# Performance work log

Hardware: AMD Instinct MI355X
Metric: run time of the kernel (lower is better)

## Reference

```python
import jax, jax.numpy as jnp
import numpy as np

B = 1024
D = 64          # embed_dim (symp == dise)
H1, H2 = 8, 8   # dsd metapath fanouts
U1, U2, U3 = 8, 8, 16  # usu metapath fanouts
NUM_SYMP = 50000
NUM_DISE = 2000
NEG_SLOPE = 0.2


def setup_inputs() -> dict:
    key = jax.random.key(0)
    ks = jax.random.split(key, 16)
    s = 0.05
    E_s = jax.random.normal(ks[0], (NUM_SYMP + 1, D), jnp.float32) * s
    E_d = jax.random.normal(ks[1], (NUM_DISE + 1, D), jnp.float32) * s
    # padding_idx=0 rows are zero in torch Embedding
    E_s = E_s.at[0].set(0.0)
    E_d = E_d.at[0].set(0.0)
    W = lambda k: jax.random.normal(k, (D, D), jnp.float32) * (1.0 / np.sqrt(D))
    return {
        "E_s": E_s,
        "E_d": E_d,
        "W_dsd_21": W(ks[2]),
        "W_dsd_22": W(ks[3]),
        "W_dsd_11": W(ks[4]),
        "W_dsd_12": W(ks[5]),
        "W_usu_3": W(ks[6]),
        "W_usu_21": W(ks[7]),
        "W_usu_22": W(ks[8]),
        "W_usu_1": W(ks[9]),
        "label": jax.random.randint(ks[10], (B,), 0, NUM_DISE + 1),
        "dsd_1": jax.random.randint(ks[11], (B, H1), 0, NUM_SYMP + 1),
        "dsd_2": jax.random.randint(ks[12], (B, H1, H2), 0, NUM_DISE + 1),
        "usu_1": jax.random.randint(ks[13], (B, U1), 0, NUM_SYMP + 1),
        "usu_2": jax.random.randint(ks[14], (B, U1, U2), 0, 10000),
        "usu_3": jax.random.randint(ks[15], (B, U1, U2, U3), 0, NUM_SYMP + 1),
    }


def _avg_real(msg, idx):
    # mean over the neighbor axis, counting only nonzero (real) neighbors;
    # zero output if all neighbors are padding (matches weight==1e8 -> 0)
    cnt = (idx != 0).sum(-1).astype(msg.dtype)
    w = jnp.where(cnt > 0, 1.0 / (cnt + 1e-8), 0.0)
    return msg.sum(-2) * w[..., None]


def _leaky(x):
    return jax.nn.leaky_relu(x, NEG_SLOPE)


def reference(E_s, E_d, W_dsd_21, W_dsd_22, W_dsd_11, W_dsd_12,
              W_usu_3, W_usu_21, W_usu_22, W_usu_1,
              label, dsd_1, dsd_2, usu_1, usu_2, usu_3):
    # ---- forward_dsd (eval mode: dropout = identity) ----
    td = E_d[label]                       # [B, D]
    es = E_s[dsd_1]                       # [B, H1, D]
    ed = E_d[dsd_2]                       # [B, H1, H2, D]
    m_sd = ed @ W_dsd_21.T + (ed * es[:, :, None, :]) @ W_dsd_22.T
    m_sd = _avg_real(m_sd, dsd_2)         # [B, H1, D]
    m_ss = es @ W_dsd_21.T                # [B, H1, D]
    emb_s1 = _leaky(m_ss + m_sd)          # [B, H1, D]
    m_ds = emb_s1 @ W_dsd_11.T + (emb_s1 * td[:, None, :]) @ W_dsd_12.T
    m_ds = _avg_real(m_ds, dsd_1)         # [B, D]
    emb_dise = _leaky(m_ds + td @ W_dsd_11.T)

    # ---- forward_usu ----
    u1 = E_s[usu_1]                       # [B, U1, D]
    s3 = E_s[usu_3]                       # [B, U1, U2, U3, D]
    m_us3 = _avg_real(s3 @ W_usu_3.T, usu_3)   # [B, U1, U2, D]
    eu2 = _leaky(m_us3)                   # [B, U1, U2, D]
    m_su = eu2 @ W_usu_21.T + (eu2 * u1[:, :, None, :]) @ W_usu_22.T
    m_su = _avg_real(m_su, usu_2)         # [B, U1, D]
    m_ss_u = u1 @ W_usu_21.T              # [B, U1, D]
    es1 = _leaky(m_ss_u + m_su)           # [B, U1, D]
    emb_user = _leaky(_avg_real(es1 @ W_usu_1.T, usu_1))  # [B, D]

    pred_score = (emb_dise * emb_user).sum(-1)  # [B]
    return pred_score
```

## Files before the change

kernel.cpp:

```cpp
#include <hip/hip_runtime.h>
#include <hip/hip_bf16.h>


typedef __attribute__((ext_vector_type(8))) short short8;
typedef __attribute__((ext_vector_type(8))) unsigned short ushort8;
typedef __attribute__((ext_vector_type(4))) float f32x4;

__device__ __forceinline__ int rfl(int v) { return __builtin_amdgcn_readfirstlane(v); }
__device__ __forceinline__ float bcastf(float v, int l) {
    return __int_as_float(__builtin_amdgcn_readlane(__float_as_int(v), l));
}
__device__ __forceinline__ float leakyf(float x) { return x >= 0.f ? x : 0.2f * x; }

__device__ __forceinline__ unsigned short bf16bits(float x) {
    __hip_bfloat16 h = __float2bfloat16(x);
    return __builtin_bit_cast(unsigned short, h);
}
__device__ __forceinline__ float bflo(unsigned int u) { return __uint_as_float(u << 16); }
__device__ __forceinline__ float bfhi(unsigned int u) { return __uint_as_float(u & 0xffff0000u); }

__device__ __forceinline__ void stage_w512(float* dst, const float* __restrict__ W, int tid) {
#pragma unroll
    for (int c = 0; c < 2; ++c) {
        int f4 = c * 512 + tid;
        int j = f4 >> 4, g = f4 & 15;
        float4 v = reinterpret_cast<const float4*>(W)[f4];
        reinterpret_cast<float4*>(dst)[(j << 4) + ((g + j) & 15)] = v;
    }
}

__device__ __forceinline__ float dot1_lds(float x, const float* w, int lane) {
    float a0 = 0.f, a1 = 0.f, a2 = 0.f, a3 = 0.f;
#pragma unroll
    for (int g = 0; g < 16; ++g) {
        float4 c = reinterpret_cast<const float4*>(w)[(lane << 4) + ((g + lane) & 15)];
        int k = 4 * g;
        a0 = fmaf(bcastf(x, k + 0), c.x, a0);
        a1 = fmaf(bcastf(x, k + 1), c.y, a1);
        a2 = fmaf(bcastf(x, k + 2), c.z, a2);
        a3 = fmaf(bcastf(x, k + 3), c.w, a3);
    }
    return (a0 + a1) + (a2 + a3);
}

__global__ __launch_bounds__(256) void k_cvt(const float* __restrict__ E_s,
                                             unsigned short* __restrict__ T) {
    int t = blockIdx.x * 256 + threadIdx.x;
    if (t >= 400008) return;
    const float4* p = reinterpret_cast<const float4*>(E_s) + (size_t)t * 2;
    float4 a = p[0], b = p[1];
    ushort8 o;
    o[0] = bf16bits(a.x); o[1] = bf16bits(a.y); o[2] = bf16bits(a.z); o[3] = bf16bits(a.w);
    o[4] = bf16bits(b.x); o[5] = bf16bits(b.y); o[6] = bf16bits(b.z); o[7] = bf16bits(b.w);
    *(reinterpret_cast<ushort8*>(T) + t) = o;
}

#define XP 72

__device__ __forceinline__ f32x4 pair_mfma(
    const unsigned short* sXs, const unsigned short* sXm,
    const unsigned short* sWb1, const unsigned short* sWb2,
    int arow, int brow, int quad)
{
    const int ab = arow * XP + quad * 8;
    const int bb = brow * XP + quad * 8;
    short8 as0 = *(const short8*)(sXs + ab);
    short8 as1 = *(const short8*)(sXs + ab + 32);
    short8 am0 = *(const short8*)(sXm + ab);
    short8 am1 = *(const short8*)(sXm + ab + 32);
    short8 b10 = *(const short8*)(sWb1 + bb);
    short8 b11 = *(const short8*)(sWb1 + bb + 32);
    short8 b20 = *(const short8*)(sWb2 + bb);
    short8 b21 = *(const short8*)(sWb2 + bb + 32);
    f32x4 acc = {0.f, 0.f, 0.f, 0.f};
    acc = __builtin_amdgcn_mfma_f32_16x16x32_bf16(as0, b10, acc, 0, 0, 0);
    acc = __builtin_amdgcn_mfma_f32_16x16x32_bf16(as1, b11, acc, 0, 0, 0);
    acc = __builtin_amdgcn_mfma_f32_16x16x32_bf16(am0, b20, acc, 0, 0, 0);
    acc = __builtin_amdgcn_mfma_f32_16x16x32_bf16(am1, b21, acc, 0, 0, 0);
    return acc;
}

__global__ __launch_bounds__(512, 6) void k_main(
    const float* __restrict__ E_s, const unsigned short* __restrict__ Ebf,
    const float* __restrict__ E_d,
    const float* __restrict__ W21, const float* __restrict__ W22,
    const float* __restrict__ W11, const float* __restrict__ W12,
    const float* __restrict__ W3, const float* __restrict__ W21u,
    const float* __restrict__ W22u, const float* __restrict__ W1u,
    const int* __restrict__ label, const int* __restrict__ dsd_1,
    const int* __restrict__ dsd_2, const int* __restrict__ usu_1,
    const int* __restrict__ usu_2, const int* __restrict__ usu_3,
    float* __restrict__ emb_dise, float* __restrict__ emb_user)
{
    __shared__ float4 smraw[2560];
    const int tid = threadIdx.x, lane = tid & 63, w = rfl(tid >> 6);
    const int m_ = lane & 15, quad = lane >> 4;

    if (blockIdx.x < 1024) {
        const int b = blockIdx.x;
        unsigned short* sXb   = (unsigned short*)smraw;
        unsigned short* sW3b  = sXb + 4608;
        unsigned short* sW21b = sW3b + 4608;
        unsigned short* sW22b = sW21b + 4608;
        float* sA2  = (float*)(sW22b + 4608);
        float* sES1 = sA2 + 512;
        unsigned short* sXs = sXb;
        unsigned short* sXm = sXb + 16 * XP;

        const int sub = lane >> 4, cg = lane & 15;

        int idv[8];
#pragma unroll
        for (int i = 0; i < 8; ++i)
            idv[i] = usu_3[((size_t)(b * 64 + w * 8 + i)) * 16 + cg];

        {
            int row = tid >> 3, c0 = (tid & 7) << 3;
            const float* p3 = W3 + row * 64 + c0;
            const float* p1 = W21u + row * 64 + c0;
            const float* p2 = W22u + row * 64 + c0;
#pragma unroll
            for (int i = 0; i < 8; ++i) {
                sW3b[row * XP + c0 + i]  = bf16bits(p3[i]);
                sW21b[row * XP + c0 + i] = bf16bits(p1[i]);
                sW22b[row * XP + c0 + i] = bf16bits(p2[i]);
            }
        }

#pragma unroll 2
        for (int i = 0; i < 8; ++i) {
            int ql = w * 8 + i;
            unsigned long long nzm = __ballot(idv[i] != 0) & 0xFFFFull;
            int cnt = (int)__popcll(nzm);
            float wgt = cnt > 0 ? 1.f / ((float)cnt + 1e-8f) : 0.f;
            float a0 = 0.f, a1 = 0.f, a2 = 0.f, a3 = 0.f;
#pragma unroll
            for (int k = 0; k < 4; ++k) {
                int id = __shfl(idv[i], k * 4 + sub, 64);
                uint2 v = *reinterpret_cast<const uint2*>(Ebf + (size_t)id * 64 + cg * 4);
                a0 += bflo(v.x); a1 += bfhi(v.x);
                a2 += bflo(v.y); a3 += bfhi(v.y);
            }
            a0 += __shfl_xor(a0, 16, 64); a1 += __shfl_xor(a1, 16, 64);
            a2 += __shfl_xor(a2, 16, 64); a3 += __shfl_xor(a3, 16, 64);
            a0 += __shfl_xor(a0, 32, 64); a1 += __shfl_xor(a1, 32, 64);
            a2 += __shfl_xor(a2, 32, 64); a3 += __shfl_xor(a3, 32, 64);
            a0 *= wgt; a1 *= wgt; a2 *= wgt; a3 *= wgt;
            unsigned int p0 = ((unsigned int)bf16bits(a1) << 16) | bf16bits(a0);
            unsigned int p1 = ((unsigned int)bf16bits(a3) << 16) | bf16bits(a2);
            if (sub == 0) {
                uint2 st; st.x = p0; st.y = p1;
                *reinterpret_cast<uint2*>(sXb + ql * XP + cg * 4) = st;
            }
        }
        __syncthreads();

        {
            const int wt = w >> 1, J0 = (w & 1) * 2;
            const int base = (16 * wt + m_) * XP + quad * 8;
            short8 a0 = *(const short8*)(sXb + base);
            short8 a1 = *(const short8*)(sXb + base + 32);
            int cp0 = 0, cp1 = 0;
            const int* m2 = usu_2 + (b * 8 + 2 * wt) * 8;
#pragma unroll
            for (int u = 0; u < 8; ++u) { cp0 += (m2[u] != 0); cp1 += (m2[u + 8] != 0); }
            float wg0 = cp0 > 0 ? 1.f / ((float)cp0 + 1e-8f) : 0.f;
            float wg1 = cp1 > 0 ? 1.f / ((float)cp1 + 1e-8f) : 0.f;
#pragma unroll
            for (int jj = 0; jj < 2; ++jj) {
                int J = J0 + jj;
                const int wb = (16 * J + m_) * XP + quad * 8;
                short8 b0 = *(const short8*)(sW3b + wb);
                short8 b1 = *(const short8*)(sW3b + wb + 32);
                f32x4 acc = {0.f, 0.f, 0.f, 0.f};
                acc = __builtin_amdgcn_mfma_f32_16x16x32_bf16(a0, b0, acc, 0, 0, 0);
                acc = __builtin_amdgcn_mfma_f32_16x16x32_bf16(a1, b1, acc, 0, 0, 0);
                float t = leakyf(acc[0]) + leakyf(acc[1]) + leakyf(acc[2]) + leakyf(acc[3]);
                t += __shfl_xor(t, 16, 64);
                if (quad == 0) sA2[(2 * wt + 0) * 64 + J * 16 + m_] = t * wg0;
                if (quad == 2) sA2[(2 * wt + 1) * 64 + J * 16 + m_] = t * wg1;
            }
        }
        __syncthreads();

        {
            int p = w;
            float x = sA2[p * 64 + lane];
            float u1e = E_s[(size_t)usu_1[b * 8 + p] * 64 + lane];
            sXs[p * XP + lane] = bf16bits(x + u1e);
            sXm[p * XP + lane] = bf16bits(x * u1e);
        }
        __syncthreads();

        if (w < 4) {
            f32x4 acc = pair_mfma(sXs, sXm, sW21b, sW22b, m_, 16 * w + m_, quad);
            if (quad < 2) {
#pragma unroll
                for (int r = 0; r < 4; ++r)
                    sES1[(quad * 4 + r) * 64 + w * 16 + m_] = leakyf(acc[r]);
            }
        }
        __syncthreads();

        stage_w512((float*)sW21b, W1u, tid);
        __syncthreads();

        if (w == 0) {
            float sE = 0.f; int cnt = 0;
            const int* u1i = usu_1 + b * 8;
#pragma unroll
            for (int h = 0; h < 8; ++h) {
                sE += sES1[h * 64 + lane];
                cnt += (u1i[h] != 0);
            }
            float wgt = cnt > 0 ? 1.f / ((float)cnt + 1e-8f) : 0.f;
            float eu = leakyf(dot1_lds(sE * wgt, (float*)sW21b, lane));
            emb_user[(size_t)b * 64 + lane] = eu;
        }
    } else {
        const int b0 = (blockIdx.x - 1024) * 4;
        unsigned short* sXs   = (unsigned short*)smraw;
        unsigned short* sXm   = sXs + 2304;
        unsigned short* sW21b = sXm + 2304;
        unsigned short* sW22b = sW21b + 4608;
        float* sS1 = (float*)(sW22b + 4608);

        {
            int row = tid >> 3, c0 = (tid & 7) << 3;
            const float* p1 = W21 + row * 64 + c0;
            const float* p2 = W22 + row * 64 + c0;
#pragma unroll
            for (int i = 0; i < 8; ++i) {
                sW21b[row * XP + c0 + i] = bf16bits(p1[i]);
                sW22b[row * XP + c0 + i] = bf16bits(p2[i]);
            }
        }

#pragma unroll
        for (int i = 0; i < 4; ++i) {
            int rl = w * 4 + i;
            int row = b0 * 8 + rl;
            int is = dsd_1[row];
            float es = E_s[(size_t)is * 64 + lane];
            const int* d2 = dsd_2 + row * 8;
            float sA = 0.f; int cnt = 0;
#pragma unroll
            for (int h = 0; h < 8; ++h) {
                int id = d2[h];
                cnt += (id != 0);
                sA += E_d[(size_t)id * 64 + lane];
            }
            float wgt = cnt > 0 ? 1.f / ((float)cnt + 1e-8f) : 0.f;
            float A = sA * wgt;
            sXs[rl * XP + lane] = bf16bits(A + es);
            sXm[rl * XP + lane] = bf16bits(A * es);
        }
        __syncthreads();

        {
            const int Mt = w >> 2, J = w & 3;
            f32x4 acc = pair_mfma(sXs, sXm, sW21b, sW22b,
                                  16 * Mt + m_, 16 * J + m_, quad);
#pragma unroll
            for (int r = 0; r < 4; ++r)
                sS1[(16 * Mt + quad * 4 + r) * 64 + J * 16 + m_] = leakyf(acc[r]);
        }
        __syncthreads();

        if (w < 4) {
            int bb = b0 + w;
            float sE = 0.f; int cnt = 0;
            const int* d1 = dsd_1 + bb * 8;
#pragma unroll
            for (int h = 0; h < 8; ++h) {
                sE += sS1[(w * 8 + h) * 64 + lane];
                cnt += (d1[h] != 0);
            }
            float wgt = cnt > 0 ? 1.f / ((float)cnt + 1e-8f) : 0.f;
            float A3 = sE * wgt;
            float td = E_d[(size_t)label[bb] * 64 + lane];
            sXs[w * XP + lane] = bf16bits(A3 + td);
            sXm[w * XP + lane] = bf16bits(A3 * td);
        } else {
            int t2 = tid - 256;
            int row = t2 >> 2, c0 = (t2 & 3) << 4;
            const float* p1 = W11 + row * 64 + c0;
            const float* p2 = W12 + row * 64 + c0;
#pragma unroll
            for (int i = 0; i < 16; ++i) {
                sW21b[row * XP + c0 + i] = bf16bits(p1[i]);
                sW22b[row * XP + c0 + i] = bf16bits(p2[i]);
            }
        }
        __syncthreads();

        if (w < 4) {
            f32x4 acc = pair_mfma(sXs, sXm, sW21b, sW22b, m_, 16 * w + m_, quad);
            if (quad == 0) {
#pragma unroll
                for (int r = 0; r < 4; ++r)
                    emb_dise[(size_t)(b0 + r) * 64 + w * 16 + m_] = leakyf(acc[r]);
            }
        }
    }
}

__global__ __launch_bounds__(256) void k_dot(const float* __restrict__ ed,
                                             const float* __restrict__ eu,
                                             float* __restrict__ out) {
    const int lane = threadIdx.x & 63;
    const int b = rfl((int)((blockIdx.x * blockDim.x + threadIdx.x) >> 6));
    float pr = ed[(size_t)b * 64 + lane] * eu[(size_t)b * 64 + lane];
#pragma unroll
    for (int off = 32; off > 0; off >>= 1) pr += __shfl_down(pr, off, 64);
    if (lane == 0) out[b] = pr;
}

extern "C" void kernel_launch(void* const* d_in, const int* in_sizes, int n_in,
                              void* d_out, int out_size, void* d_ws, size_t ws_size,
                              hipStream_t stream) {
    const float* E_s  = (const float*)d_in[0];
    const float* E_d  = (const float*)d_in[1];
    const float* W_dsd_21 = (const float*)d_in[2];
    const float* W_dsd_22 = (const float*)d_in[3];
    const float* W_dsd_11 = (const float*)d_in[4];
    const float* W_dsd_12 = (const float*)d_in[5];
    const float* W_usu_3  = (const float*)d_in[6];
    const float* W_usu_21 = (const float*)d_in[7];
    const float* W_usu_22 = (const float*)d_in[8];
    const float* W_usu_1  = (const float*)d_in[9];
    const int* label = (const int*)d_in[10];
    const int* dsd_1 = (const int*)d_in[11];
    const int* dsd_2 = (const int*)d_in[12];
    const int* usu_1 = (const int*)d_in[13];
    const int* usu_2 = (const int*)d_in[14];
    const int* usu_3 = (const int*)d_in[15];
    float* out = (float*)d_out;

    unsigned short* Ebf = (unsigned short*)d_ws;
    float* emb_dise = (float*)((char*)d_ws + 6400128);
    float* emb_user = emb_dise + 1024 * 64;

    k_cvt<<<1563, 256, 0, stream>>>(E_s, Ebf);
    k_main<<<1280, 512, 0, stream>>>(E_s, Ebf, E_d,
                                     W_dsd_21, W_dsd_22, W_dsd_11, W_dsd_12,
                                     W_usu_3, W_usu_21, W_usu_22, W_usu_1,
                                     label, dsd_1, dsd_2, usu_1, usu_2, usu_3,
                                     emb_dise, emb_user);
    k_dot<<<256, 256, 0, stream>>>(emb_dise, emb_user, out);
}
```

Measured before the change: 115.6 us.

## Restructure usu block: per-wave W3 MFMA, bf16 W1u staging, MFMA final projection

The usu branch now stages W1u as bf16 in LDS up front instead of restaging fp32 W1u over W21 late. Each wave runs the W3 MFMA on its own eight gathered rows with a wave-local count, removing one block barrier. The final emb_user projection uses an MFMA on four waves in place of the single-wave readlane dot product. This raises LDS use per block, which may lower occupancy, and rounds the final projection to bf16.

```diff
diff --git a/kernel.cpp b/kernel.cpp
--- a/kernel.cpp
+++ b/kernel.cpp
@@ -7,9 +7,6 @@
 typedef __attribute__((ext_vector_type(4))) float f32x4;
 
 __device__ __forceinline__ int rfl(int v) { return __builtin_amdgcn_readfirstlane(v); }
-__device__ __forceinline__ float bcastf(float v, int l) {
-    return __int_as_float(__builtin_amdgcn_readlane(__float_as_int(v), l));
-}
 __device__ __forceinline__ float leakyf(float x) { return x >= 0.f ? x : 0.2f * x; }
 
 __device__ __forceinline__ unsigned short bf16bits(float x) {
@@ -18,30 +15,6 @@
 }
 __device__ __forceinline__ float bflo(unsigned int u) { return __uint_as_float(u << 16); }
 __device__ __forceinline__ float bfhi(unsigned int u) { return __uint_as_float(u & 0xffff0000u); }
-
-__device__ __forceinline__ void stage_w512(float* dst, const float* __restrict__ W, int tid) {
-#pragma unroll
-    for (int c = 0; c < 2; ++c) {
-        int f4 = c * 512 + tid;
-        int j = f4 >> 4, g = f4 & 15;
-        float4 v = reinterpret_cast<const float4*>(W)[f4];
-        reinterpret_cast<float4*>(dst)[(j << 4) + ((g + j) & 15)] = v;
-    }
-}
-
-__device__ __forceinline__ float dot1_lds(float x, const float* w, int lane) {
-    float a0 = 0.f, a1 = 0.f, a2 = 0.f, a3 = 0.f;
-#pragma unroll
-    for (int g = 0; g < 16; ++g) {
-        float4 c = reinterpret_cast<const float4*>(w)[(lane << 4) + ((g + lane) & 15)];
-        int k = 4 * g;
-        a0 = fmaf(bcastf(x, k + 0), c.x, a0);
-        a1 = fmaf(bcastf(x, k + 1), c.y, a1);
-        a2 = fmaf(bcastf(x, k + 2), c.z, a2);
-        a3 = fmaf(bcastf(x, k + 3), c.w, a3);
-    }
-    return (a0 + a1) + (a2 + a3);
-}
 
 __global__ __launch_bounds__(256) void k_cvt(const float* __restrict__ E_s,
                                              unsigned short* __restrict__ T) {
@@ -92,44 +65,52 @@
     const int* __restrict__ usu_2, const int* __restrict__ usu_3,
     float* __restrict__ emb_dise, float* __restrict__ emb_user)
 {
-    __shared__ float4 smraw[2560];
+    __shared__ float4 smraw[3296];
     const int tid = threadIdx.x, lane = tid & 63, w = rfl(tid >> 6);
     const int m_ = lane & 15, quad = lane >> 4;
 
     if (blockIdx.x < 1024) {
         const int b = blockIdx.x;
-        unsigned short* sXb   = (unsigned short*)smraw;
-        unsigned short* sW3b  = sXb + 4608;
+        unsigned short* sX    = (unsigned short*)smraw;
+        unsigned short* sW3b  = sX + 4608;
         unsigned short* sW21b = sW3b + 4608;
         unsigned short* sW22b = sW21b + 4608;
-        float* sA2  = (float*)(sW22b + 4608);
-        float* sES1 = sA2 + 512;
-        unsigned short* sXs = sXb;
-        unsigned short* sXm = sXb + 16 * XP;
+        unsigned short* sW1ub = sW22b + 4608;
+        unsigned short* sP    = sW1ub + 4608;
+        float* sA2  = (float*)(sP + 2304);
+        float* sES1 = sA2;
 
         const int sub = lane >> 4, cg = lane & 15;
+        const int p = b * 8 + w;
 
         int idv[8];
 #pragma unroll
         for (int i = 0; i < 8; ++i)
-            idv[i] = usu_3[((size_t)(b * 64 + w * 8 + i)) * 16 + cg];
+            idv[i] = usu_3[((size_t)p * 8 + i) * 16 + cg];
+
+        int mu = usu_2[p * 8 + (lane & 7)];
+        unsigned long long mm = __ballot(mu != 0);
+        int cnt2 = (int)__popcll(mm & 0xFFull);
+        float wg = cnt2 > 0 ? 1.f / ((float)cnt2 + 1e-8f) : 0.f;
 
         {
             int row = tid >> 3, c0 = (tid & 7) << 3;
             const float* p3 = W3 + row * 64 + c0;
             const float* p1 = W21u + row * 64 + c0;
             const float* p2 = W22u + row * 64 + c0;
+            const float* pf = W1u + row * 64 + c0;
 #pragma unroll
             for (int i = 0; i < 8; ++i) {
                 sW3b[row * XP + c0 + i]  = bf16bits(p3[i]);
                 sW21b[row * XP + c0 + i] = bf16bits(p1[i]);
                 sW22b[row * XP + c0 + i] = bf16bits(p2[i]);
-            }
-        }
+                sW1ub[row * XP + c0 + i] = bf16bits(pf[i]);
+            }
+        }
+        __syncthreads();
 
 #pragma unroll 2
         for (int i = 0; i < 8; ++i) {
-            int ql = w * 8 + i;
             unsigned long long nzm = __ballot(idv[i] != 0) & 0xFFFFull;
             int cnt = (int)__popcll(nzm);
             float wgt = cnt > 0 ? 1.f / ((float)cnt + 1e-8f) : 0.f;
@@ -146,63 +127,49 @@
             a0 += __shfl_xor(a0, 32, 64); a1 += __shfl_xor(a1, 32, 64);
             a2 += __shfl_xor(a2, 32, 64); a3 += __shfl_xor(a3, 32, 64);
             a0 *= wgt; a1 *= wgt; a2 *= wgt; a3 *= wgt;
-            unsigned int p0 = ((unsigned int)bf16bits(a1) << 16) | bf16bits(a0);
-            unsigned int p1 = ((unsigned int)bf16bits(a3) << 16) | bf16bits(a2);
+            unsigned int q0 = ((unsigned int)bf16bits(a1) << 16) | bf16bits(a0);
+            unsigned int q1 = ((unsigned int)bf16bits(a3) << 16) | bf16bits(a2);
             if (sub == 0) {
-                uint2 st; st.x = p0; st.y = p1;
-                *reinterpret_cast<uint2*>(sXb + ql * XP + cg * 4) = st;
-            }
-        }
-        __syncthreads();
-
-        {
-            const int wt = w >> 1, J0 = (w & 1) * 2;
-            const int base = (16 * wt + m_) * XP + quad * 8;
-            short8 a0 = *(const short8*)(sXb + base);
-            short8 a1 = *(const short8*)(sXb + base + 32);
-            int cp0 = 0, cp1 = 0;
-            const int* m2 = usu_2 + (b * 8 + 2 * wt) * 8;
-#pragma unroll
-            for (int u = 0; u < 8; ++u) { cp0 += (m2[u] != 0); cp1 += (m2[u + 8] != 0); }
-            float wg0 = cp0 > 0 ? 1.f / ((float)cp0 + 1e-8f) : 0.f;
-            float wg1 = cp1 > 0 ? 1.f / ((float)cp1 + 1e-8f) : 0.f;
-#pragma unroll
-            for (int jj = 0; jj < 2; ++jj) {
-                int J = J0 + jj;
+                uint2 st; st.x = q0; st.y = q1;
+                *reinterpret_cast<uint2*>(sX + (w * 8 + i) * XP + cg * 4) = st;
+            }
+        }
+        {
+            const int abase = (w * 8 + (m_ & 7)) * XP + quad * 8;
+            short8 xa0 = *(const short8*)(sX + abase);
+            short8 xa1 = *(const short8*)(sX + abase + 32);
+#pragma unroll
+            for (int J = 0; J < 4; ++J) {
                 const int wb = (16 * J + m_) * XP + quad * 8;
-                short8 b0 = *(const short8*)(sW3b + wb);
-                short8 b1 = *(const short8*)(sW3b + wb + 32);
+                short8 wb0 = *(const short8*)(sW3b + wb);
+                short8 wb1 = *(const short8*)(sW3b + wb + 32);
                 f32x4 acc = {0.f, 0.f, 0.f, 0.f};
-                acc = __builtin_amdgcn_mfma_f32_16x16x32_bf16(a0, b0, acc, 0, 0, 0);
-                acc = __builtin_amdgcn_mfma_f32_16x16x32_bf16(a1, b1, acc, 0, 0, 0);
+                acc = __builtin_amdgcn_mfma_f32_16x16x32_bf16(xa0, wb0, acc, 0, 0, 0);
+                acc = __builtin_amdgcn_mfma_f32_16x16x32_bf16(xa1, wb1, acc, 0, 0, 0);
                 float t = leakyf(acc[0]) + leakyf(acc[1]) + leakyf(acc[2]) + leakyf(acc[3]);
                 t += __shfl_xor(t, 16, 64);
-                if (quad == 0) sA2[(2 * wt + 0) * 64 + J * 16 + m_] = t * wg0;
-                if (quad == 2) sA2[(2 * wt + 1) * 64 + J * 16 + m_] = t * wg1;
-            }
-        }
-        __syncthreads();
-
-        {
-            int p = w;
-            float x = sA2[p * 64 + lane];
-            float u1e = E_s[(size_t)usu_1[b * 8 + p] * 64 + lane];
-            sXs[p * XP + lane] = bf16bits(x + u1e);
-            sXm[p * XP + lane] = bf16bits(x * u1e);
+                t *= wg;
+                if (lane < 16) sA2[w * 64 + J * 16 + lane] = t;
+            }
+        }
+        __syncthreads();
+
+        {
+            float x = sA2[w * 64 + lane];
+            float u1e = E_s[(size_t)usu_1[b * 8 + w] * 64 + lane];
+            sP[w * XP + lane]        = bf16bits(x + u1e);
+            sP[(16 + w) * XP + lane] = bf16bits(x * u1e);
         }
         __syncthreads();
 
         if (w < 4) {
-            f32x4 acc = pair_mfma(sXs, sXm, sW21b, sW22b, m_, 16 * w + m_, quad);
+            f32x4 acc = pair_mfma(sP, sP + 16 * XP, sW21b, sW22b, m_, 16 * w + m_, quad);
             if (quad < 2) {
 #pragma unroll
                 for (int r = 0; r < 4; ++r)
                     sES1[(quad * 4 + r) * 64 + w * 16 + m_] = leakyf(acc[r]);
             }
         }
-        __syncthreads();
-
-        stage_w512((float*)sW21b, W1u, tid);
         __syncthreads();
 
         if (w == 0) {
@@ -214,8 +181,22 @@
                 cnt += (u1i[h] != 0);
             }
             float wgt = cnt > 0 ? 1.f / ((float)cnt + 1e-8f) : 0.f;
-            float eu = leakyf(dot1_lds(sE * wgt, (float*)sW21b, lane));
-            emb_user[(size_t)b * 64 + lane] = eu;
+            sP[lane] = bf16bits(sE * wgt);
+        }
+        __syncthreads();
+
+        if (w < 4) {
+            const int fb = m_ * XP + quad * 8;
+            short8 fa0 = *(const short8*)(sP + fb);
+            short8 fa1 = *(const short8*)(sP + fb + 32);
+            const int bb = (16 * w + m_) * XP + quad * 8;
+            short8 fb0 = *(const short8*)(sW1ub + bb);
+            short8 fb1 = *(const short8*)(sW1ub + bb + 32);
+            f32x4 acc = {0.f, 0.f, 0.f, 0.f};
+            acc = __builtin_amdgcn_mfma_f32_16x16x32_bf16(fa0, fb0, acc, 0, 0, 0);
+            acc = __builtin_amdgcn_mfma_f32_16x16x32_bf16(fa1, fb1, acc, 0, 0, 0);
+            if (quad == 0)
+                emb_user[(size_t)b * 64 + w * 16 + m_] = leakyf(acc[0]);
         }
     } else {
         const int b0 = (blockIdx.x - 1024) * 4;
```

Result: slower. 119.7 us (+3.5%).

## Move dsd branch into bf16 conversion kernel and use MFMA for final usu projection

Applied to the files above, without the earlier changes.

The dsd-path blocks are moved out of the main kernel into the bf16 table-conversion kernel, so they run alongside the conversion instead of after it, and the main kernel only handles the usu path. The final W_usu_1 projection switches from a readlane-based fp32 dot product to a bf16 MFMA, with W1u staged in LDS at block start next to the other weights. This drops a barrier and the weight restaging step, but raises LDS use per block in k_main and adds bf16 rounding to the last projection.

```diff
diff --git a/kernel.cpp b/kernel.cpp
--- a/kernel.cpp
+++ b/kernel.cpp
@@ -7,9 +7,6 @@
 typedef __attribute__((ext_vector_type(4))) float f32x4;
 
 __device__ __forceinline__ int rfl(int v) { return __builtin_amdgcn_readfirstlane(v); }
-__device__ __forceinline__ float bcastf(float v, int l) {
-    return __int_as_float(__builtin_amdgcn_readlane(__float_as_int(v), l));
-}
 __device__ __forceinline__ float leakyf(float x) { return x >= 0.f ? x : 0.2f * x; }
 
 __device__ __forceinline__ unsigned short bf16bits(float x) {
@@ -18,42 +15,6 @@
 }
 __device__ __forceinline__ float bflo(unsigned int u) { return __uint_as_float(u << 16); }
 __device__ __forceinline__ float bfhi(unsigned int u) { return __uint_as_float(u & 0xffff0000u); }
-
-__device__ __forceinline__ void stage_w512(float* dst, const float* __restrict__ W, int tid) {
-#pragma unroll
-    for (int c = 0; c < 2; ++c) {
-        int f4 = c * 512 + tid;
-        int j = f4 >> 4, g = f4 & 15;
-        float4 v = reinterpret_cast<const float4*>(W)[f4];
-        reinterpret_cast<float4*>(dst)[(j << 4) + ((g + j) & 15)] = v;
-    }
-}
-
-__device__ __forceinline__ float dot1_lds(float x, const float* w, int lane) {
-    float a0 = 0.f, a1 = 0.f, a2 = 0.f, a3 = 0.f;
-#pragma unroll
-    for (int g = 0; g < 16; ++g) {
-        float4 c = reinterpret_cast<const float4*>(w)[(lane << 4) + ((g + lane) & 15)];
-        int k = 4 * g;
-        a0 = fmaf(bcastf(x, k + 0), c.x, a0);
-        a1 = fmaf(bcastf(x, k + 1), c.y, a1);
-        a2 = fmaf(bcastf(x, k + 2), c.z, a2);
-        a3 = fmaf(bcastf(x, k + 3), c.w, a3);
-    }
-    return (a0 + a1) + (a2 + a3);
-}
-
-__global__ __launch_bounds__(256) void k_cvt(const float* __restrict__ E_s,
-                                             unsigned short* __restrict__ T) {
-    int t = blockIdx.x * 256 + threadIdx.x;
-    if (t >= 400008) return;
-    const float4* p = reinterpret_cast<const float4*>(E_s) + (size_t)t * 2;
-    float4 a = p[0], b = p[1];
-    ushort8 o;
-    o[0] = bf16bits(a.x); o[1] = bf16bits(a.y); o[2] = bf16bits(a.z); o[3] = bf16bits(a.w);
-    o[4] = bf16bits(b.x); o[5] = bf16bits(b.y); o[6] = bf16bits(b.z); o[7] = bf16bits(b.w);
-    *(reinterpret_cast<ushort8*>(T) + t) = o;
-}
 
 #define XP 72
 
@@ -80,228 +41,260 @@
     return acc;
 }
 
+__global__ __launch_bounds__(512, 6) void k_pre(
+    const float* __restrict__ E_s, const float* __restrict__ E_d,
+    const float* __restrict__ W21, const float* __restrict__ W22,
+    const float* __restrict__ W11, const float* __restrict__ W12,
+    const int* __restrict__ label, const int* __restrict__ dsd_1,
+    const int* __restrict__ dsd_2,
+    unsigned short* __restrict__ Ebf, float* __restrict__ emb_dise)
+{
+    __shared__ float4 smraw[2240];
+    const int tid = threadIdx.x;
+
+    if (blockIdx.x >= 256) {
+        int t = (blockIdx.x - 256) * 512 + tid;
+        if (t >= 400008) return;
+        const float4* p = reinterpret_cast<const float4*>(E_s) + (size_t)t * 2;
+        float4 a = p[0], b = p[1];
+        ushort8 o;
+        o[0] = bf16bits(a.x); o[1] = bf16bits(a.y); o[2] = bf16bits(a.z); o[3] = bf16bits(a.w);
+        o[4] = bf16bits(b.x); o[5] = bf16bits(b.y); o[6] = bf16bits(b.z); o[7] = bf16bits(b.w);
+        *(reinterpret_cast<ushort8*>(Ebf) + t) = o;
+        return;
+    }
+
+    const int lane = tid & 63, w = rfl(tid >> 6);
+    const int m_ = lane & 15, quad = lane >> 4;
+    const int b0 = blockIdx.x * 4;
+    unsigned short* sXs   = (unsigned short*)smraw;
+    unsigned short* sXm   = sXs + 2304;
+    unsigned short* sW21b = sXm + 2304;
+    unsigned short* sW22b = sW21b + 4608;
+    float* sS1 = (float*)(sW22b + 4608);
+
+    {
+        int row = tid >> 3, c0 = (tid & 7) << 3;
+        const float* p1 = W21 + row * 64 + c0;
+        const float* p2 = W22 + row * 64 + c0;
+#pragma unroll
+        for (int i = 0; i < 8; ++i) {
+            sW21b[row * XP + c0 + i] = bf16bits(p1[i]);
+            sW22b[row * XP + c0 + i] = bf16bits(p2[i]);
+        }
+    }
+
+#pragma unroll
+    for (int i = 0; i < 4; ++i) {
+        int rl = w * 4 + i;
+        int row = b0 * 8 + rl;
+        int is = dsd_1[row];
+        float es = E_s[(size_t)is * 64 + lane];
+        const int* d2 = dsd_2 + row * 8;
+        float sA = 0.f; int cnt = 0;
+#pragma unroll
+        for (int h = 0; h < 8; ++h) {
+            int id = d2[h];
+            cnt += (id != 0);
+            sA += E_d[(size_t)id * 64 + lane];
+        }
+        float wgt = cnt > 0 ? 1.f / ((float)cnt + 1e-8f) : 0.f;
+        float A = sA * wgt;
+        sXs[rl * XP + lane] = bf16bits(A + es);
+        sXm[rl * XP + lane] = bf16bits(A * es);
+    }
+    __syncthreads();
+
+    {
+        const int Mt = w >> 2, J = w & 3;
+        f32x4 acc = pair_mfma(sXs, sXm, sW21b, sW22b,
+                              16 * Mt + m_, 16 * J + m_, quad);
+#pragma unroll
+        for (int r = 0; r < 4; ++r)
+            sS1[(16 * Mt + quad * 4 + r) * 64 + J * 16 + m_] = leakyf(acc[r]);
+    }
+    __syncthreads();
+
+    if (w < 4) {
+        int bb = b0 + w;
+        float sE = 0.f; int cnt = 0;
+        const int* d1 = dsd_1 + bb * 8;
+#pragma unroll
+        for (int h = 0; h < 8; ++h) {
+            sE += sS1[(w * 8 + h) * 64 + lane];
+            cnt += (d1[h] != 0);
+        }
+        float wgt = cnt > 0 ? 1.f / ((float)cnt + 1e-8f) : 0.f;
+        float A3 = sE * wgt;
+        float td = E_d[(size_t)label[bb] * 64 + lane];
+        sXs[w * XP + lane] = bf16bits(A3 + td);
+        sXm[w * XP + lane] = bf16bits(A3 * td);
+    } else {
+        int t2 = tid - 256;
+        int row = t2 >> 2, c0 = (t2 & 3) << 4;
+        const float* p1 = W11 + row * 64 + c0;
+        const float* p2 = W12 + row * 64 + c0;
+#pragma unroll
+        for (int i = 0; i < 16; ++i) {
+            sW21b[row * XP + c0 + i] = bf16bits(p1[i]);
+            sW22b[row * XP + c0 + i] = bf16bits(p2[i]);
+        }
+    }
+    __syncthreads();
+
+    if (w < 4) {
+        f32x4 acc = pair_mfma(sXs, sXm, sW21b, sW22b, m_, 16 * w + m_, quad);
+        if (quad == 0) {
+#pragma unroll
+            for (int r = 0; r < 4; ++r)
+                emb_dise[(size_t)(b0 + r) * 64 + w * 16 + m_] = leakyf(acc[r]);
+        }
+    }
+}
+
 __global__ __launch_bounds__(512, 6) void k_main(
     const float* __restrict__ E_s, const unsigned short* __restrict__ Ebf,
-    const float* __restrict__ E_d,
-    const float* __restrict__ W21, const float* __restrict__ W22,
-    const float* __restrict__ W11, const float* __restrict__ W12,
     const float* __restrict__ W3, const float* __restrict__ W21u,
     const float* __restrict__ W22u, const float* __restrict__ W1u,
-    const int* __restrict__ label, const int* __restrict__ dsd_1,
-    const int* __restrict__ dsd_2, const int* __restrict__ usu_1,
-    const int* __restrict__ usu_2, const int* __restrict__ usu_3,
-    float* __restrict__ emb_dise, float* __restrict__ emb_user)
+    const int* __restrict__ usu_1, const int* __restrict__ usu_2,
+    const int* __restrict__ usu_3, float* __restrict__ emb_user)
 {
-    __shared__ float4 smraw[2560];
+    __shared__ float4 smraw[3136];
     const int tid = threadIdx.x, lane = tid & 63, w = rfl(tid >> 6);
     const int m_ = lane & 15, quad = lane >> 4;
-
-    if (blockIdx.x < 1024) {
-        const int b = blockIdx.x;
-        unsigned short* sXb   = (unsigned short*)smraw;
-        unsigned short* sW3b  = sXb + 4608;
-        unsigned short* sW21b = sW3b + 4608;
-        unsigned short* sW22b = sW21b + 4608;
-        float* sA2  = (float*)(sW22b + 4608);
-        float* sES1 = sA2 + 512;
-        unsigned short* sXs = sXb;
-        unsigned short* sXm = sXb + 16 * XP;
-
-        const int sub = lane >> 4, cg = lane & 15;
-
-        int idv[8];
-#pragma unroll
-        for (int i = 0; i < 8; ++i)
-            idv[i] = usu_3[((size_t)(b * 64 + w * 8 + i)) * 16 + cg];
-
-        {
-            int row = tid >> 3, c0 = (tid & 7) << 3;
-            const float* p3 = W3 + row * 64 + c0;
-            const float* p1 = W21u + row * 64 + c0;
-            const float* p2 = W22u + row * 64 + c0;
-#pragma unroll
-            for (int i = 0; i < 8; ++i) {
-                sW3b[row * XP + c0 + i]  = bf16bits(p3[i]);
-                sW21b[row * XP + c0 + i] = bf16bits(p1[i]);
-                sW22b[row * XP + c0 + i] = bf16bits(p2[i]);
-            }
-        }
+    const int b = blockIdx.x;
+
+    unsigned short* sXb   = (unsigned short*)smraw;
+    unsigned short* sW3b  = sXb + 4608;
+    unsigned short* sW21b = sW3b + 4608;
+    unsigned short* sW22b = sW21b + 4608;
+    unsigned short* sW1ub = sW22b + 4608;
+    float* sA2  = (float*)(sW1ub + 4608);
+    float* sES1 = sA2 + 512;
+    unsigned short* sXs = sXb;
+    unsigned short* sXm = sXb + 16 * XP;
+
+    const int sub = lane >> 4, cg = lane & 15;
+
+    int idv[8];
+#pragma unroll
+    for (int i = 0; i < 8; ++i)
+        idv[i] = usu_3[((size_t)(b * 64 + w * 8 + i)) * 16 + cg];
+
+    {
+        int row = tid >> 3, c0 = (tid & 7) << 3;
+        const float* p3 = W3 + row * 64 + c0;
+        const float* p1 = W21u + row * 64 + c0;
+        const float* p2 = W22u + row * 64 + c0;
+        const float* pf = W1u + row * 64 + c0;
+#pragma unroll
+        for (int i = 0; i < 8; ++i) {
+            sW3b[row * XP + c0 + i]  = bf16bits(p3[i]);
+            sW21b[row * XP + c0 + i] = bf16bits(p1[i]);
+            sW22b[row * XP + c0 + i] = bf16bits(p2[i]);
+            sW1ub[row * XP + c0 + i] = bf16bits(pf[i]);
+        }
+    }
 
 #pragma unroll 2
-        for (int i = 0; i < 8; ++i) {
-            int ql = w * 8 + i;
-            unsigned long long nzm = __ballot(idv[i] != 0) & 0xFFFFull;
-            int cnt = (int)__popcll(nzm);
-            float wgt = cnt > 0 ? 1.f / ((float)cnt + 1e-8f) : 0.f;
-            float a0 = 0.f, a1 = 0.f, a2 = 0.f, a3 = 0.f;
-#pragma unroll
-            for (int k = 0; k < 4; ++k) {
-                int id = __shfl(idv[i], k * 4 + sub, 64);
-                uint2 v = *reinterpret_cast<const uint2*>(Ebf + (size_t)id * 64 + cg * 4);
-                a0 += bflo(v.x); a1 += bfhi(v.x);
-                a2 += bflo(v.y); a3 += bfhi(v.y);
-            }
-            a0 += __shfl_xor(a0, 16, 64); a1 += __shfl_xor(a1, 16, 64);
-            a2 += __shfl_xor(a2, 16, 64); a3 += __shfl_xor(a3, 16, 64);
-            a0 += __shfl_xor(a0, 32, 64); a1 += __shfl_xor(a1, 32, 64);
-            a2 += __shfl_xor(a2, 32, 64); a3 += __shfl_xor(a3, 32, 64);
-            a0 *= wgt; a1 *= wgt; a2 *= wgt; a3 *= wgt;
-            unsigned int p0 = ((unsigned int)bf16bits(a1) << 16) | bf16bits(a0);
-            unsigned int p1 = ((unsigned int)bf16bits(a3) << 16) | bf16bits(a2);
-            if (sub == 0) {
-                uint2 st; st.x = p0; st.y = p1;
-                *reinterpret_cast<uint2*>(sXb + ql * XP + cg * 4) = st;
-            }
-        }
-        __syncthreads();
-
-        {
-            const int wt = w >> 1, J0 = (w & 1) * 2;
-            const int base = (16 * wt + m_) * XP + quad * 8;
-            short8 a0 = *(const short8*)(sXb + base);
-            short8 a1 = *(const short8*)(sXb + base + 32);
-            int cp0 = 0, cp1 = 0;
-            const int* m2 = usu_2 + (b * 8 + 2 * wt) * 8;
-#pragma unroll
-            for (int u = 0; u < 8; ++u) { cp0 += (m2[u] != 0); cp1 += (m2[u + 8] != 0); }
-            float wg0 = cp0 > 0 ? 1.f / ((float)cp0 + 1e-8f) : 0.f;
-            float wg1 = cp1 > 0 ? 1.f / ((float)cp1 + 1e-8f) : 0.f;
-#pragma unroll
-            for (int jj = 0; jj < 2; ++jj) {
-                int J = J0 + jj;
-                const int wb = (16 * J + m_) * XP + quad * 8;
-                short8 b0 = *(const short8*)(sW3b + wb);
-                short8 b1 = *(const short8*)(sW3b + wb + 32);
-                f32x4 acc = {0.f, 0.f, 0.f, 0.f};
-                acc = __builtin_amdgcn_mfma_f32_16x16x32_bf16(a0, b0, acc, 0, 0, 0);
-                acc = __builtin_amdgcn_mfma_f32_16x16x32_bf16(a1, b1, acc, 0, 0, 0);
-                float t = leakyf(acc[0]) + leakyf(acc[1]) + leakyf(acc[2]) + leakyf(acc[3]);
-                t += __shfl_xor(t, 16, 64);
-                if (quad == 0) sA2[(2 * wt + 0) * 64 + J * 16 + m_] = t * wg0;
-                if (quad == 2) sA2[(2 * wt + 1) * 64 + J * 16 + m_] = t * wg1;
-            }
-        }
-        __syncthreads();
-
-        {
-            int p = w;
-            float x = sA2[p * 64 + lane];
-            float u1e = E_s[(size_t)usu_1[b * 8 + p] * 64 + lane];
-            sXs[p * XP + lane] = bf16bits(x + u1e);
-            sXm[p * XP + lane] = bf16bits(x * u1e);
-        }
-        __syncthreads();
-
-        if (w < 4) {
-            f32x4 acc = pair_mfma(sXs, sXm, sW21b, sW22b, m_, 16 * w + m_, quad);
-            if (quad < 2) {
-#pragma unroll
-                for (int r = 0; r < 4; ++r)
-                    sES1[(quad * 4 + r) * 64 + w * 16 + m_] = leakyf(acc[r]);
-            }
-        }
-        __syncthreads();
-
-        stage_w512((float*)sW21b, W1u, tid);
-        __syncthreads();
-
-        if (w == 0) {
-            float sE = 0.f; int cnt = 0;
-            const int* u1i = usu_1 + b * 8;
-#pragma unroll
-            for (int h = 0; h < 8; ++h) {
-                sE += sES1[h * 64 + lane];
-                cnt += (u1i[h] != 0);
-            }
-            float wgt = cnt > 0 ? 1.f / ((float)cnt + 1e-8f) : 0.f;
-            float eu = leakyf(dot1_lds(sE * wgt, (float*)sW21b, lane));
-            emb_user[(size_t)b * 64 + lane] = eu;
-        }
-    } else {
-        const int b0 = (blockIdx.x - 1024) * 4;
-        unsigned short* sXs   = (unsigned short*)smraw;
-        unsigned short* sXm   = sXs + 2304;
-        unsigned short* sW21b = sXm + 2304;
-        unsigned short* sW22b = sW21b + 4608;
-        float* sS1 = (float*)(sW22b + 4608);
-
-        {
-            int row = tid >> 3, c0 = (tid & 7) << 3;
-            const float* p1 = W21 + row * 64 + c0;
-            const float* p2 = W22 + row * 64 + c0;
-#pragma unroll
-            for (int i = 0; i < 8; ++i) {
-                sW21b[row * XP + c0 + i] = bf16bits(p1[i]);
-                sW22b[row * XP + c0 + i] = bf16bits(p2[i]);
-            }
-        }
-
-#pragma unroll
-        for (int i = 0; i < 4; ++i) {
-            int rl = w * 4 + i;
-            int row = b0 * 8 + rl;
-            int is = dsd_1[row];
-            float es = E_s[(size_t)is * 64 + lane];
-            const int* d2 = dsd_2 + row * 8;
-            float sA = 0.f; int cnt = 0;
-#pragma unroll
-            for (int h = 0; h < 8; ++h) {
-                int id = d2[h];
-                cnt += (id != 0);
-                sA += E_d[(size_t)id * 64 + lane];
-            }
-            float wgt = cnt > 0 ? 1.f / ((float)cnt + 1e-8f) : 0.f;
-            float A = sA * wgt;
-            sXs[rl * XP + lane] = bf16bits(A + es);
-            sXm[rl * XP + lane] = bf16bits(A * es);
-        }
-        __syncthreads();
-
-        {
-            const int Mt = w >> 2, J = w & 3;
-            f32x4 acc = pair_mfma(sXs, sXm, sW21b, sW22b,
-                                  16 * Mt + m_, 16 * J + m_, quad);
+    for (int i = 0; i < 8; ++i) {
+        int ql = w * 8 + i;
+        unsigned long long nzm = __ballot(idv[i] != 0) & 0xFFFFull;
+        int cnt = (int)__popcll(nzm);
+        float wgt = cnt > 0 ? 1.f / ((float)cnt + 1e-8f) : 0.f;
+        float a0 = 0.f, a1 = 0.f, a2 = 0.f, a3 = 0.f;
+#pragma unroll
+        for (int k = 0; k < 4; ++k) {
+            int id = __shfl(idv[i], k * 4 + sub, 64);
+            uint2 v = *reinterpret_cast<const uint2*>(Ebf + (size_t)id * 64 + cg * 4);
+            a0 += bflo(v.x); a1 += bfhi(v.x);
+            a2 += bflo(v.y); a3 += bfhi(v.y);
+        }
+        a0 += __shfl_xor(a0, 16, 64); a1 += __shfl_xor(a1, 16, 64);
+        a2 += __shfl_xor(a2, 16, 64); a3 += __shfl_xor(a3, 16, 64);
+        a0 += __shfl_xor(a0, 32, 64); a1 += __shfl_xor(a1, 32, 64);
+        a2 += __shfl_xor(a2, 32, 64); a3 += __shfl_xor(a3, 32, 64);
+        a0 *= wgt; a1 *= wgt; a2 *= wgt; a3 *= wgt;
+        unsigned int q0 = ((unsigned int)bf16bits(a1) << 16) | bf16bits(a0);
+        unsigned int q1 = ((unsigned int)bf16bits(a3) << 16) | bf16bits(a2);
+        if (sub == 0) {
+            uint2 st; st.x = q0; st.y = q1;
+            *reinterpret_cast<uint2*>(sXb + ql * XP + cg * 4) = st;
+        }
+    }
+    __syncthreads();
+
+    {
+        const int wt = w >> 1, J0 = (w & 1) * 2;
+        const int base = (16 * wt + m_) * XP + quad * 8;
+        short8 a0 = *(const short8*)(sXb + base);
+        short8 a1 = *(const short8*)(sXb + base + 32);
+        int cp0 = 0, cp1 = 0;
+        const int* m2 = usu_2 + (b * 8 + 2 * wt) * 8;
+#pragma unroll
+        for (int u = 0; u < 8; ++u) { cp0 += (m2[u] != 0); cp1 += (m2[u + 8] != 0); }
+        float wg0 = cp0 > 0 ? 1.f / ((float)cp0 + 1e-8f) : 0.f;
+        float wg1 = cp1 > 0 ? 1.f / ((float)cp1 + 1e-8f) : 0.f;
+#pragma unroll
+        for (int jj = 0; jj < 2; ++jj) {
+            int J = J0 + jj;
+            const int wb = (16 * J + m_) * XP + quad * 8;
+            short8 b0 = *(const short8*)(sW3b + wb);
+            short8 b1 = *(const short8*)(sW3b + wb + 32);
+            f32x4 acc = {0.f, 0.f, 0.f, 0.f};
+            acc = __builtin_amdgcn_mfma_f32_16x16x32_bf16(a0, b0, acc, 0, 0, 0);
+            acc = __builtin_amdgcn_mfma_f32_16x16x32_bf16(a1, b1, acc, 0, 0, 0);
+            float t = leakyf(acc[0]) + leakyf(acc[1]) + leakyf(acc[2]) + leakyf(acc[3]);
+            t += __shfl_xor(t, 16, 64);
+            if (quad == 0) sA2[(2 * wt + 0) * 64 + J * 16 + m_] = t * wg0;
+            if (quad == 2) sA2[(2 * wt + 1) * 64 + J * 16 + m_] = t * wg1;
+        }
+    }
+    __syncthreads();
+
+    {
+        float x = sA2[w * 64 + lane];
+        float u1e = E_s[(size_t)usu_1[b * 8 + w] * 64 + lane];
+        sXs[w * XP + lane] = bf16bits(x + u1e);
+        sXm[w * XP + lane] = bf16bits(x * u1e);
+    }
+    __syncthreads();
+
+    if (w < 4) {
+        f32x4 acc = pair_mfma(sXs, sXm, sW21b, sW22b, m_, 16 * w + m_, quad);
+        if (quad < 2) {
 #pragma unroll
             for (int r = 0; r < 4; ++r)
-                sS1[(16 * Mt + quad * 4 + r) * 64 + J * 16 + m_] = leakyf(acc[r]);
-        }
-        __syncthreads();
-
-        if (w < 4) {
-            int bb = b0 + w;
-            float sE = 0.f; int cnt = 0;
-            const int* d1 = dsd_1 + bb * 8;
-#pragma unroll
-            for (int h = 0; h < 8; ++h) {
-                sE += sS1[(w * 8 + h) * 64 + lane];
-                cnt += (d1[h] != 0);
-            }
-            float wgt = cnt > 0 ? 1.f / ((float)cnt + 1e-8f) : 0.f;
-            float A3 = sE * wgt;
-            float td = E_d[(size_t)label[bb] * 64 + lane];
-            sXs[w * XP + lane] = bf16bits(A3 + td);
-            sXm[w * XP + lane] = bf16bits(A3 * td);
-        } else {
-            int t2 = tid - 256;
-            int row = t2 >> 2, c0 = (t2 & 3) << 4;
-            const float* p1 = W11 + row * 64 + c0;
-            const float* p2 = W12 + row * 64 + c0;
-#pragma unroll
-            for (int i = 0; i < 16; ++i) {
-                sW21b[row * XP + c0 + i] = bf16bits(p1[i]);
-                sW22b[row * XP + c0 + i] = bf16bits(p2[i]);
-            }
-        }
-        __syncthreads();
-
-        if (w < 4) {
-            f32x4 acc = pair_mfma(sXs, sXm, sW21b, sW22b, m_, 16 * w + m_, quad);
-            if (quad == 0) {
-#pragma unroll
-                for (int r = 0; r < 4; ++r)
-                    emb_dise[(size_t)(b0 + r) * 64 + w * 16 + m_] = leakyf(acc[r]);
-            }
-        }
+                sES1[(quad * 4 + r) * 64 + w * 16 + m_] = leakyf(acc[r]);
+        }
+    }
+    __syncthreads();
+
+    if (w == 0) {
+        float sE = 0.f; int cnt = 0;
+        const int* u1i = usu_1 + b * 8;
+#pragma unroll
+        for (int h = 0; h < 8; ++h) {
+            sE += sES1[h * 64 + lane];
+            cnt += (u1i[h] != 0);
+        }
+        float wgt = cnt > 0 ? 1.f / ((float)cnt + 1e-8f) : 0.f;
+        sXb[lane] = bf16bits(sE * wgt);
+    }
+    __syncthreads();
+
+    if (w < 4) {
+        const int fb = m_ * XP + quad * 8;
+        short8 fa0 = *(const short8*)(sXb + fb);
+        short8 fa1 = *(const short8*)(sXb + fb + 32);
+        const int bb = (16 * w + m_) * XP + quad * 8;
+        short8 fb0 = *(const short8*)(sW1ub + bb);
+        short8 fb1 = *(const short8*)(sW1ub + bb + 32);
+        f32x4 acc = {0.f, 0.f, 0.f, 0.f};
+        acc = __builtin_amdgcn_mfma_f32_16x16x32_bf16(fa0, fb0, acc, 0, 0, 0);
+        acc = __builtin_amdgcn_mfma_f32_16x16x32_bf16(fa1, fb1, acc, 0, 0, 0);
+        if (quad == 0)
+            emb_user[(size_t)b * 64 + w * 16 + m_] = leakyf(acc[0]);
     }
 }
 
@@ -341,11 +334,9 @@
     float* emb_dise = (float*)((char*)d_ws + 6400128);
     float* emb_user = emb_dise + 1024 * 64;
 
-    k_cvt<<<1563, 256, 0, stream>>>(E_s, Ebf);
-    k_main<<<1280, 512, 0, stream>>>(E_s, Ebf, E_d,
-                                     W_dsd_21, W_dsd_22, W_dsd_11, W_dsd_12,
-                                     W_usu_3, W_usu_21, W_usu_22, W_usu_1,
-                                     label, dsd_1, dsd_2, usu_1, usu_2, usu_3,
-                                     emb_dise, emb_user);
+    k_pre<<<1038, 512, 0, stream>>>(E_s, E_d, W_dsd_21, W_dsd_22, W_dsd_11, W_dsd_12,
+                                    label, dsd_1, dsd_2, Ebf, emb_dise);
+    k_main<<<1024, 512, 0, stream>>>(E_s, Ebf, W_usu_3, W_usu_21, W_usu_22, W_usu_1,
+                                     usu_1, usu_2, usu_3, emb_user);
     k_dot<<<256, 256, 0, stream>>>(emb_dise, emb_user, out);
 }
```

Result: slower. 120.3 us (+4.1%).
